# Kernel optimization log

Hardware: AMD Instinct MI355X
Metric: run time of the kernel (lower is better)

The kernel has to match this reference:

```python
import jax, jax.numpy as jnp
import numpy as np

K = 501   # box-filter length (conv kernel height)
P = 250   # reflect padding on each side of the time axis


def setup_inputs() -> dict:
    key = jax.random.key(0)
    k1, k2 = jax.random.split(key)
    pred = jax.random.normal(k1, (8, 16384, 128), dtype=jnp.float32)  # [B, T, C]
    # Conv2d default bias init: U(-b, b) with b = 1/sqrt(fan_in) = 1/sqrt(501)
    b = 1.0 / np.sqrt(K)
    bias = jax.random.uniform(k2, (1,), dtype=jnp.float32, minval=-b, maxval=b)
    return {"pred": pred, "bias": bias}


def reference(pred, bias):
    # Reflect-pad the time axis, then compute the 501-wide moving sum via a
    # prefix-sum (O(N) instead of O(N*K) dense conv) — same math as the
    # all-ones Conv2d kernel with reflect padding.
    x = jnp.pad(pred, ((0, 0), (P, P), (0, 0)), mode="reflect")  # [B, T+2P, C]
    c = jnp.cumsum(x, axis=1)
    c = jnp.concatenate([jnp.zeros_like(c[:, :1, :]), c], axis=1)  # [B, T+2P+1, C]
    win_sum = c[:, K:, :] - c[:, :-K, :]                            # [B, T, C]
    smoothed = (win_sum + bias[0]) / K  # conv output (ones weights + bias) / kernel_size
    return jnp.maximum(pred, smoothed)
```

## Files before the change

### kernel.cpp

```cpp
#include <hip/hip_runtime.h>


constexpr int B    = 8;
constexpr int T    = 16384;
constexpr int C    = 128;
constexpr int K    = 501;
constexpr int Pp   = 250;
constexpr int CHN  = 16;
constexpr int NCG  = C / CHN;
constexpr int NSEG = 8;
constexpr int SEGR = T / NSEG;
constexpr int RING = 1024;
constexpr int CHK  = 64;
constexpr int NC   = (SEGR + 512) / CHK;
constexpr int PRO  = 12;

__device__ __forceinline__ int ridx(int j) {
    j = (j < 0) ? -j : j;
    return (j >= T) ? (2 * T - 2 - j) : j;
}

__device__ __forceinline__ void dma16(const float* g, float* l) {
    __builtin_amdgcn_global_load_lds(
        (const __attribute__((address_space(1))) void*)g,
        (__attribute__((address_space(3))) void*)l, 16, 0, 0);
}
__device__ __forceinline__ void dma4(const float* g, float* l) {
    __builtin_amdgcn_global_load_lds(
        (const __attribute__((address_space(1))) void*)g,
        (__attribute__((address_space(3))) void*)l, 4, 0, 0);
}

__global__ __launch_bounds__(64) void smoother_kernel(
    const float* __restrict__ pred, const float* __restrict__ bias,
    float* __restrict__ out) {
    __shared__ float ring[RING * CHN];

    const int b   = blockIdx.x & 7;
    const int cg  = (blockIdx.x >> 3) & 7;
    const int seg = blockIdx.x >> 6;
    const int g0  = seg * SEGR;
    const int jstart = g0 - 256;

    const int lane = threadIdx.x & 63;
    const int q    = lane >> 4;
    const int ch   = lane & 15;

    const float* pb = pred + (size_t)b * T * C;
    float*       ob = out  + (size_t)b * T * C + cg * CHN + ch;

    const float rk  = 1.0f / (float)K;
    const float brk = bias[0] * rk;

    auto stage = [&](int m) {
        const int j0  = jstart + m * CHK;
        const int ph0 = (m * CHK) & (RING - 1);
        if (j0 >= 0 && j0 + CHK - 1 < T) {
            #pragma unroll
            for (int i = 0; i < 4; ++i) {
                const float* g = pb + (size_t)(j0 + 16 * i + (lane >> 2)) * C
                               + cg * CHN + (lane & 3) * 4;
                dma16(g, &ring[(size_t)(ph0 + 16 * i) * CHN]);
            }
        } else {
            #pragma unroll
            for (int i = 0; i < 16; ++i) {
                const int jr = ridx(j0 + 4 * i + (lane >> 4));
                const float* g = pb + (size_t)jr * C + cg * CHN + (lane & 15);
                dma4(g, &ring[(size_t)(ph0 + 4 * i) * CHN]);
            }
        }
    };

    for (int m = 0; m < PRO; ++m) stage(m);

    float acc = 0.0f;
    #pragma unroll 5
    for (int i = 0; i < 125; ++i)
        acc += ring[(size_t)(6 + 4 * i + q) * CHN + ch];
    float a2 = acc + __shfl_xor(acc, 16);
    float S  = a2 + __shfl_xor(a2, 32);
    S += ring[(size_t)506 * CHN + ch];

    int rn = 507 + q;
    int ro = 6   + q;
    int rc = 256 + q;
    int my_t = g0 + q;

    for (int k = 0; k < SEGR / CHK; ++k) {
        #pragma unroll 4
        for (int i = 0; i < CHK / 4; ++i) {
            const float vn = ring[(size_t)rn * CHN + ch];
            const float vo = ring[(size_t)ro * CHN + ch];
            const float vc = ring[(size_t)rc * CHN + ch];
            const float d  = vn - vo;
            float x = d;
            const float u1 = __shfl_up(x, 16); if (lane >= 16) x += u1;
            const float u2 = __shfl_up(x, 32); if (lane >= 32) x += u2;
            const float tot = __shfl(x, 48 + ch);
            const float sm  = S + (x - d);
            const float o   = fmaxf(vc, fmaf(sm, rk, brk));
            __builtin_nontemporal_store(o, &ob[(size_t)my_t * C]);
            S += tot;
            rn = (rn + 4) & (RING - 1);
            ro = (ro + 4) & (RING - 1);
            rc = (rc + 4) & (RING - 1);
            my_t += 4;
        }
        if (PRO + k < NC) stage(PRO + k);
    }
}

extern "C" void kernel_launch(void* const* d_in, const int* in_sizes, int n_in,
                              void* d_out, int out_size, void* d_ws, size_t ws_size,
                              hipStream_t stream) {
    const float* pred = (const float*)d_in[0];
    const float* bias = (const float*)d_in[1];
    float*       out  = (float*)d_out;

    const int blocks = B * NCG * NSEG;
    smoother_kernel<<<blocks, 64, 0, stream>>>(pred, bias, out);
}
```

Before: 149.1 us.

## Halve channels per block and replace shuffle scan with per-lane strided window sums

Each block now handles 8 channels instead of 16, which doubles the block count to 1024. The 64 lanes are split into 8 time-offset groups of 8 channels. Each lane advances its running sum by 8 rows per step, accumulating 8 new-minus-old differences from LDS. This replaces the per-step shuffle prefix scan across quarter-waves, removing the shuffle latency chain but adding more LDS reads per output. A shadow region past the ring end is filled so that strided reads never need wrap-around masks inside the unrolled loop.

```diff
diff --git a/kernel.cpp b/kernel.cpp
--- a/kernel.cpp
+++ b/kernel.cpp
@@ -5,15 +5,14 @@
 constexpr int T    = 16384;
 constexpr int C    = 128;
 constexpr int K    = 501;
-constexpr int Pp   = 250;
-constexpr int CHN  = 16;
-constexpr int NCG  = C / CHN;
+constexpr int CHN  = 8;
 constexpr int NSEG = 8;
 constexpr int SEGR = T / NSEG;
 constexpr int RING = 1024;
+constexpr int SHAD = 64;
 constexpr int CHK  = 64;
-constexpr int NC   = (SEGR + 512) / CHK;
 constexpr int PRO  = 12;
+constexpr int NC   = 40;
 
 __device__ __forceinline__ int ridx(int j) {
     j = (j < 0) ? -j : j;
@@ -31,83 +30,89 @@
         (__attribute__((address_space(3))) void*)l, 4, 0, 0);
 }
 
-__global__ __launch_bounds__(64) void smoother_kernel(
+__global__ __launch_bounds__(64, 1) void smoother_kernel(
     const float* __restrict__ pred, const float* __restrict__ bias,
     float* __restrict__ out) {
-    __shared__ float ring[RING * CHN];
+    __shared__ float ring[(RING + SHAD) * CHN];
 
     const int b   = blockIdx.x & 7;
-    const int cg  = (blockIdx.x >> 3) & 7;
-    const int seg = blockIdx.x >> 6;
+    const int cg  = (blockIdx.x >> 3) & 15;
+    const int seg = blockIdx.x >> 7;
     const int g0  = seg * SEGR;
     const int jstart = g0 - 256;
 
     const int lane = threadIdx.x & 63;
-    const int q    = lane >> 4;
-    const int ch   = lane & 15;
+    const int o    = lane >> 3;
+    const int ch   = lane & 7;
 
-    const float* pb = pred + (size_t)b * T * C;
-    float*       ob = out  + (size_t)b * T * C + cg * CHN + ch;
+    const float* pb = pred + (size_t)b * T * C + cg * CHN;
+
+    auto writeChunk = [&](int j0, int tp) {
+        if (j0 >= 0 && j0 + CHK <= T) {
+            #pragma unroll
+            for (int i = 0; i < 2; ++i) {
+                const float* g = pb + (size_t)(j0 + 32 * i + (lane >> 1)) * C
+                               + (lane & 1) * 4;
+                dma16(g, &ring[(tp + 32 * i) * CHN]);
+            }
+        } else {
+            #pragma unroll
+            for (int i = 0; i < 8; ++i) {
+                const int jr = ridx(j0 + 8 * i + (lane >> 3));
+                dma4(pb + (size_t)jr * C + (lane & 7),
+                     &ring[(tp + 8 * i) * CHN]);
+            }
+        }
+    };
+    auto stage = [&](int m) {
+        const int ph0 = (m * CHK) & (RING - 1);
+        const int j0  = jstart + m * CHK;
+        writeChunk(j0, ph0);
+        if (ph0 == 0) writeChunk(j0, RING);
+    };
+
+    for (int m = 0; m < PRO; ++m) stage(m);
 
     const float rk  = 1.0f / (float)K;
     const float brk = bias[0] * rk;
 
-    auto stage = [&](int m) {
-        const int j0  = jstart + m * CHK;
-        const int ph0 = (m * CHK) & (RING - 1);
-        if (j0 >= 0 && j0 + CHK - 1 < T) {
+    float acc = 0.f;
+    for (int i = 6 + o; i <= 506; i += 8)
+        acc += ring[i * CHN + ch];
+    acc += __shfl_xor(acc, 8);
+    acc += __shfl_xor(acc, 16);
+    acc += __shfl_xor(acc, 32);
+    float S = acc;
+    #pragma unroll
+    for (int i = 1; i < 8; ++i) {
+        const float e = ring[(506 + i) * CHN + ch] - ring[(5 + i) * CHN + ch];
+        S += (i <= o) ? e : 0.f;
+    }
+
+    int iN = (507 + o) * CHN + ch;
+    int iO = (6   + o) * CHN + ch;
+    int iC = (256 + o) * CHN + ch;
+    float* op = out + (size_t)b * T * C + (size_t)(g0 + o) * C + cg * CHN + ch;
+
+    int ms = PRO;
+    for (int k = 0; k < SEGR / CHK; ++k) {
+        #pragma unroll
+        for (int i2 = 0; i2 < CHK / 8; ++i2) {
+            const int off = i2 * 64;
+            float d = 0.f;
             #pragma unroll
-            for (int i = 0; i < 4; ++i) {
-                const float* g = pb + (size_t)(j0 + 16 * i + (lane >> 2)) * C
-                               + cg * CHN + (lane & 3) * 4;
-                dma16(g, &ring[(size_t)(ph0 + 16 * i) * CHN]);
-            }
-        } else {
-            #pragma unroll
-            for (int i = 0; i < 16; ++i) {
-                const int jr = ridx(j0 + 4 * i + (lane >> 4));
-                const float* g = pb + (size_t)jr * C + cg * CHN + (lane & 15);
-                dma4(g, &ring[(size_t)(ph0 + 4 * i) * CHN]);
-            }
+            for (int j = 0; j < 8; ++j)
+                d += ring[iN + off + 8 * j] - ring[iO + off + 8 * j];
+            const float vc = ring[iC + off];
+            const float sm = fmaf(S, rk, brk);
+            __builtin_nontemporal_store(fmaxf(vc, sm), op);
+            S += d;
+            op += 8 * C;
         }
-    };
-
-    for (int m = 0; m < PRO; ++m) stage(m);
-
-    float acc = 0.0f;
-    #pragma unroll 5
-    for (int i = 0; i < 125; ++i)
-        acc += ring[(size_t)(6 + 4 * i + q) * CHN + ch];
-    float a2 = acc + __shfl_xor(acc, 16);
-    float S  = a2 + __shfl_xor(a2, 32);
-    S += ring[(size_t)506 * CHN + ch];
-
-    int rn = 507 + q;
-    int ro = 6   + q;
-    int rc = 256 + q;
-    int my_t = g0 + q;
-
-    for (int k = 0; k < SEGR / CHK; ++k) {
-        #pragma unroll 4
-        for (int i = 0; i < CHK / 4; ++i) {
-            const float vn = ring[(size_t)rn * CHN + ch];
-            const float vo = ring[(size_t)ro * CHN + ch];
-            const float vc = ring[(size_t)rc * CHN + ch];
-            const float d  = vn - vo;
-            float x = d;
-            const float u1 = __shfl_up(x, 16); if (lane >= 16) x += u1;
-            const float u2 = __shfl_up(x, 32); if (lane >= 32) x += u2;
-            const float tot = __shfl(x, 48 + ch);
-            const float sm  = S + (x - d);
-            const float o   = fmaxf(vc, fmaf(sm, rk, brk));
-            __builtin_nontemporal_store(o, &ob[(size_t)my_t * C]);
-            S += tot;
-            rn = (rn + 4) & (RING - 1);
-            ro = (ro + 4) & (RING - 1);
-            rc = (rc + 4) & (RING - 1);
-            my_t += 4;
-        }
-        if (PRO + k < NC) stage(PRO + k);
+        iN += 512; iN = (iN >= RING * CHN) ? iN - RING * CHN : iN;
+        iO += 512; iO = (iO >= RING * CHN) ? iO - RING * CHN : iO;
+        iC += 512; iC = (iC >= RING * CHN) ? iC - RING * CHN : iC;
+        if (ms < NC) { stage(ms); ++ms; }
     }
 }
 
@@ -118,6 +123,6 @@
     const float* bias = (const float*)d_in[1];
     float*       out  = (float*)d_out;
 
-    const int blocks = B * NCG * NSEG;
+    const int blocks = B * (C / CHN) * NSEG;
     smoother_kernel<<<blocks, 64, 0, stream>>>(pred, bias, out);
 }
```

Result: slower. 152.4 us (+2.2%).
